# Optimization experiments

Measured on AMD Instinct MI355X. Metric: run time of the kernel, lower is better.

## Reference

```python
import jax, jax.numpy as jnp
import numpy as np

N = 100000
F = 128
H = 128
E = 3200000


def setup_inputs() -> dict:
    key = jax.random.key(0)
    ks = jax.random.split(key, 12)
    s = 1.0 / np.sqrt(F)
    return {
        "x": jax.random.normal(ks[0], (N, F), jnp.float32),
        "edge_weight": jax.random.uniform(ks[1], (E,), jnp.float32),
        "p": jax.random.normal(ks[2], (F,), jnp.float32) * s,
        "w_ih": jax.random.normal(ks[3], (3 * F, F), jnp.float32) * s,
        "w_hh": jax.random.normal(ks[4], (3 * F, F), jnp.float32) * s,
        "b_ih": jax.random.normal(ks[5], (3 * F,), jnp.float32) * s,
        "b_hh": jax.random.normal(ks[6], (3 * F,), jnp.float32) * s,
        "w0": jax.random.normal(ks[7], (F, F), jnp.float32) * s,
        "w_lin": jax.random.normal(ks[8], (H, F), jnp.float32) * s,
        "b_lin": jax.random.normal(ks[9], (H,), jnp.float32) * s,
        "edge_index": jax.random.randint(ks[10], (2, E), 0, N, jnp.int64),
    }


def _evolve_gcnh(x, edge_index, edge_weight, p, w_ih, w_hh, b_ih, b_hh, w0):
    n_nodes, f = x.shape
    # --- TopKPooling: keep k = f nodes by learned projection score ---
    score = jnp.tanh((x @ p) / jnp.linalg.norm(p))  # [N]
    top_scores, idx = jax.lax.top_k(score, f)
    x_tilde = x[idx] * top_scores[:, None]  # [F, F]
    # --- single GRU step (batch=F, input=F): hidden state = GCN weight ---
    gi = x_tilde @ w_ih.T + b_ih  # [F, 3F]
    gh = w0 @ w_hh.T + b_hh       # [F, 3F]
    i_r, i_z, i_n = jnp.split(gi, 3, axis=-1)
    h_r, h_z, h_n = jnp.split(gh, 3, axis=-1)
    r = jax.nn.sigmoid(i_r + h_r)
    z = jax.nn.sigmoid(i_z + h_z)
    n = jnp.tanh(i_n + r * h_n)
    W = (1.0 - z) * n + z * w0  # evolved weight [F, F]
    # --- GCNConv with fixed W: sym-normalized sparse aggregation ---
    src, dst = edge_index[0], edge_index[1]
    loop = jnp.arange(n_nodes)
    src = jnp.concatenate([src, loop])
    dst = jnp.concatenate([dst, loop])
    ew = jnp.concatenate([edge_weight, jnp.ones((n_nodes,), x.dtype)])
    deg = jax.ops.segment_sum(ew, dst, num_segments=n_nodes)
    dinv = jnp.where(deg > 0, jax.lax.rsqrt(deg), 0.0)
    norm = dinv[src] * ew * dinv[dst]  # [E+N]
    xw = x @ W  # [N, F]
    out = jax.ops.segment_sum(norm[:, None] * xw[src], dst, num_segments=n_nodes)
    return out


def reference(x, edge_weight, p, w_ih, w_hh, b_ih, b_hh, w0, w_lin, b_lin, edge_index):
    h = _evolve_gcnh(x, edge_index, edge_weight, p, w_ih, w_hh, b_ih, b_hh, w0)
    h = jax.nn.relu(h)
    return h @ w_lin.T + b_lin
```

## Files before the change

### kernel.cpp

```cpp
#include <hip/hip_runtime.h>
#include <hip/hip_fp16.h>
#include <stdint.h>

#define FD 128
#define CAP 4096
#define PSH 8
#define NPART_MAX 512
#define NBLK1 1024
#define EBUF_MAX 4096
#define SCORE_BLKS 2048
#define TRANS_BLKS 448

static inline size_t alignup256(size_t x) { return (x + 255) & ~(size_t)255; }

struct EdgeP { int s; float w; };

typedef __attribute__((ext_vector_type(4))) float f32x4;
typedef __attribute__((ext_vector_type(8))) short bf16x8;

__device__ __forceinline__ unsigned short f32_to_bf16(float f) {
  unsigned u = __float_as_uint(f);
  u += 0x7fffu + ((u >> 16) & 1u);
  return (unsigned short)(u >> 16);
}
__device__ __forceinline__ unsigned pack_bf16(float a, float b) {
  return ((unsigned)f32_to_bf16(b) << 16) | (unsigned)f32_to_bf16(a);
}
__device__ __forceinline__ unsigned pack_f16(float a, float b) {
  unsigned short ha = __half_as_ushort(__float2half_rn(a));
  unsigned short hb = __half_as_ushort(__float2half_rn(b));
  return ((unsigned)hb << 16) | (unsigned)ha;
}
__device__ __forceinline__ float f16lo(unsigned u) {
  return __half2float(__ushort_as_half((unsigned short)(u & 0xffffu)));
}
__device__ __forceinline__ float f16hi(unsigned u) {
  return __half2float(__ushort_as_half((unsigned short)(u >> 16)));
}
__device__ __forceinline__ unsigned mono32(float f) {
  unsigned u = __float_as_uint(f);
  return (u & 0x80000000u) ? ~u : (u | 0x80000000u);
}
__device__ __forceinline__ unsigned long long mono64(double d) {
  unsigned long long b = (unsigned long long)__double_as_longlong(d);
  return (b & 0x8000000000000000ULL) ? ~b : (b | 0x8000000000000000ULL);
}

__global__ __launch_bounds__(256)
void k_front(const float* __restrict__ x, const float* __restrict__ pvec,
             double* __restrict__ dvals, unsigned* __restrict__ hist,
             unsigned short* __restrict__ xb, unsigned* __restrict__ cnt, int N,
             const int* __restrict__ dstA, unsigned* __restrict__ pcnt, int E, int NPART,
             const float* __restrict__ w_ih, const float* __restrict__ w_hh,
             const float* __restrict__ w_lin, float* __restrict__ w_ihT,
             float* __restrict__ w_hhT, unsigned short* __restrict__ wlb)
{
  int b = blockIdx.x, t = threadIdx.x;
  if (b < SCORE_BLKS) {
    int gid = b * 256 + t;
    if (gid == 0) *cnt = 0u;
    int wid = gid >> 6, lane = t & 63;
    const int nw = (SCORE_BLKS * 256) >> 6;
    double p0 = (double)pvec[lane * 2], p1 = (double)pvec[lane * 2 + 1];
    for (int n = wid; n < N; n += nw) {
      float2 xv = *(const float2*)(x + (size_t)n * FD + lane * 2);
      unsigned pk = pack_f16(xv.x, xv.y);
      *(unsigned*)(xb + (size_t)n * FD + lane * 2) = pk;
      double s = (double)xv.x * p0 + (double)xv.y * p1;
      #pragma unroll
      for (int o = 32; o > 0; o >>= 1) s += __shfl_down(s, o, 64);
      if (lane == 0) {
        dvals[n] = s;
        unsigned u = mono32((float)s);
        atomicAdd(&hist[u >> 16], 1u);
      }
    }
  } else if (b < SCORE_BLKS + NBLK1) {
    __shared__ unsigned lh[NPART_MAX];
    int bid = b - SCORE_BLKS;
    for (int i = t; i < NPART; i += 256) lh[i] = 0;
    __syncthreads();
    int chunk = (E + NBLK1 - 1) / NBLK1;
    int e0 = bid * chunk;
    int e1 = e0 + chunk; if (e1 > E) e1 = E;
    for (int e = e0 + t; e < e1; e += 256)
      atomicAdd(&lh[dstA[e] >> PSH], 1u);
    __syncthreads();
    for (int i = t; i < NPART; i += 256)
      pcnt[(size_t)i * NBLK1 + bid] = lh[i];
  } else {
    int vb = (b - SCORE_BLKS - NBLK1) * 2 + (t >> 7);
    int c = t & 127;
    if (vb < 384)      w_ihT[(size_t)c * 384 + vb]         = w_ih[(size_t)vb * 128 + c];
    else if (vb < 768) w_hhT[(size_t)c * 384 + (vb - 384)] = w_hh[(size_t)(vb - 384) * 128 + c];
    else               wlb[(size_t)(vb - 768) * 128 + c]   = f32_to_bf16(w_lin[(size_t)(vb - 768) * 128 + c]);
  }
}

__global__ __launch_bounds__(1024)
void k_mid1(const unsigned* __restrict__ hist, unsigned* __restrict__ Bthr,
            const unsigned* __restrict__ pcnt, unsigned* __restrict__ basel,
            unsigned* __restrict__ ptot)
{
  int t = threadIdx.x;
  if (blockIdx.x == 0) {
    __shared__ unsigned part[1024];
    unsigned s = 0;
    for (int i = 0; i < 64; i++) s += hist[t * 64 + i];
    part[t] = s;
    __syncthreads();
    if (t == 0) {
      unsigned cum = 0;
      int chunk = 1023;
      for (; chunk >= 0; chunk--) {
        if (cum + part[chunk] >= 128u) break;
        cum += part[chunk];
      }
      unsigned B = 0;
      if (chunk >= 0) {
        int b = chunk * 64 + 63;
        for (; b >= chunk * 64; b--) {
          cum += hist[b];
          if (cum >= 128u) break;
        }
        B = (unsigned)b;
      }
      *Bthr = B;
    }
  } else {
    __shared__ unsigned wtot[16];
    int p = blockIdx.x - 1;
    int lane = t & 63, wv = t >> 6;
    unsigned c = pcnt[(size_t)p * NBLK1 + t];
    unsigned v = c;
    #pragma unroll
    for (int d = 1; d < 64; d <<= 1) {
      unsigned u = __shfl_up(v, d, 64);
      if (lane >= d) v += u;
    }
    if (lane == 63) wtot[wv] = v;
    __syncthreads();
    unsigned add = 0;
    #pragma unroll
    for (int w = 0; w < 16; w++) if (w < wv) add += wtot[w];
    v += add;
    basel[(size_t)p * NBLK1 + t] = v - c;
    if (t == NBLK1 - 1) ptot[p] = v;
  }
}

__global__ __launch_bounds__(512)
void k_mid2(const int* __restrict__ srcA, const int* __restrict__ dstA,
            const float* __restrict__ ew, const unsigned* __restrict__ ptot,
            const unsigned* __restrict__ basel, unsigned long long* __restrict__ epk2,
            int E, int NPART,
            const double* __restrict__ dvals, const unsigned* __restrict__ Bthr,
            unsigned long long* __restrict__ ckey, unsigned* __restrict__ cidx,
            unsigned* __restrict__ cnt, int N)
{
  int t = threadIdx.x;
  if (blockIdx.x < NBLK1) {
    __shared__ unsigned long long ebuf[EBUF_MAX];
    __shared__ unsigned short pbuf[EBUF_MAX];
    __shared__ unsigned lcnt[NPART_MAX];
    __shared__ unsigned lbase[NPART_MAX];
    __shared__ unsigned cur[NPART_MAX];
    __shared__ int gbase[NPART_MAX];
    __shared__ unsigned wt1[8], wt2[8];
    int b = blockIdx.x;
    int chunk = (E + NBLK1 - 1) / NBLK1;
    int e0 = b * chunk;
    int e1 = e0 + chunk; if (e1 > E) e1 = E;
    int n = e1 - e0;

    lcnt[t] = 0;
    unsigned pt = (t < NPART) ? ptot[t] : 0u;
    __syncthreads();
    for (int e = e0 + t; e < e1; e += 512)
      atomicAdd(&lcnt[dstA[e] >> PSH], 1u);
    __syncthreads();
    int lane = t & 63, wv = t >> 6;
    unsigned c1 = lcnt[t];
    unsigned v1 = c1, v2 = pt;
    #pragma unroll
    for (int d = 1; d < 64; d <<= 1) {
      unsigned u1 = __shfl_up(v1, d, 64);
      unsigned u2 = __shfl_up(v2, d, 64);
      if (lane >= d) { v1 += u1; v2 += u2; }
    }
    if (lane == 63) { wt1[wv] = v1; wt2[wv] = v2; }
    __syncthreads();
    unsigned a1 = 0, a2 = 0;
    #pragma unroll
    for (int w = 0; w < 8; w++) if (w < wv) { a1 += wt1[w]; a2 += wt2[w]; }
    v1 += a1; v2 += a2;
    lbase[t] = v1 - c1;
    cur[t] = v1 - c1;
    gbase[t] = (t < NPART) ? ((int)(v2 - pt) + (int)basel[(size_t)t * NBLK1 + b]) : 0;
    __syncthreads();
    for (int e = e0 + t; e < e1; e += 512) {
      int d = dstA[e];
      int s = srcA[e];
      float w = ew[e];
      int p = d >> PSH;
      unsigned long long v = ((unsigned long long)__float_as_uint(w) << 32)
                           | ((unsigned long long)(unsigned)s << 8)
                           | (unsigned long long)(d & 255);
      unsigned pos = atomicAdd(&cur[p], 1u);
      ebuf[pos] = v;
      pbuf[pos] = (unsigned short)p;
    }
    __syncthreads();
    for (int j = t; j < n; j += 512) {
      int p = pbuf[j];
      epk2[gbase[p] + (j - (int)lbase[p])] = ebuf[j];
    }
  } else {
    int i = (blockIdx.x - NBLK1) * 512 + t;
    if (i >= N) return;
    unsigned B = *Bthr;
    double d = dvals[i];
    unsigned u = mono32((float)d);
    if ((u >> 16) >= B) {
      unsigned pos = atomicAdd(cnt, 1u);
      if (pos < CAP) {
        ckey[pos] = ~mono64(d);
        cidx[pos] = (unsigned)i;
      }
    }
  }
}

__global__ __launch_bounds__(512)
void k_mid3(const double* __restrict__ dvals, const float* __restrict__ pvec,
            const unsigned* __restrict__ cnt,
            const unsigned long long* __restrict__ ckey, const unsigned* __restrict__ cidx,
            unsigned* __restrict__ sel_idx, float* __restrict__ sel_ts,
            const unsigned* __restrict__ ptot, const unsigned long long* __restrict__ epk2,
            EdgeP* __restrict__ epk_out, int* __restrict__ off,
            float* __restrict__ dinv, int N, int NPART)
{
  int t = threadIdx.x;
  if (blockIdx.x == 0) {
    __shared__ unsigned long long k[CAP];
    __shared__ unsigned id[CAP];
    __shared__ double red[128];
    __shared__ double pn_sh;
    unsigned C = *cnt;
    if (C > CAP) C = CAP;
    int S = 128;
    while (S < (int)C) S <<= 1;
    for (int i = t; i < S; i += 512) {
      if (i < (int)C) { k[i] = ckey[i]; id[i] = cidx[i]; }
      else            { k[i] = ~0ULL;   id[i] = 0xFFFFFFFFu; }
    }
    __syncthreads();
    for (int kk = 2; kk <= S; kk <<= 1) {
      for (int j = kk >> 1; j > 0; j >>= 1) {
        for (int i = t; i < S; i += 512) {
          int q = i ^ j;
          if (q > i) {
            bool up = ((i & kk) == 0);
            bool g = (k[i] > k[q]) || (k[i] == k[q] && id[i] > id[q]);
            if (g == up) {
              unsigned long long tk = k[i]; k[i] = k[q]; k[q] = tk;
              unsigned ti = id[i]; id[i] = id[q]; id[q] = ti;
            }
          }
        }
        __syncthreads();
      }
    }
    if (t < 128) { double v = (double)pvec[t]; red[t] = v * v; }
    __syncthreads();
    if (t == 0) {
      double s = 0.0;
      for (int i = 0; i < 128; i++) s += red[i];
      pn_sh = sqrt(s);
    }
    __syncthreads();
    if (t < 128) {
      unsigned n = id[t];
      sel_idx[t] = n;
      sel_ts[t] = (float)tanh(dvals[n] / pn_sh);
    }
  } else {
    int p = blockIdx.x - 1;
    int lane = t & 63, wv = t >> 6;
    __shared__ unsigned ws[8];
    __shared__ unsigned wt[4];
    __shared__ unsigned lcnt[256];
    __shared__ float ldeg[256];
    unsigned a = (t < p) ? ptot[t] : 0u;
    #pragma unroll
    for (int d = 32; d > 0; d >>= 1) a += __shfl_xor(a, d, 64);
    if (lane == 0) ws[wv] = a;
    __syncthreads();
    unsigned bu = 0;
    #pragma unroll
    for (int w = 0; w < 8; w++) bu += ws[w];
    int beg = (int)bu;
    int end = beg + (int)ptot[p];

    int n0 = p << PSH;
    int nn = N - n0; if (nn > 256) nn = 256;
    if (t < 256) { lcnt[t] = 0; ldeg[t] = 0.f; }
    __syncthreads();
    for (int i = beg + t; i < end; i += 512) {
      unsigned long long v = epk2[i];
      int ln = (int)(v & 255u);
      float w = __uint_as_float((unsigned)(v >> 32));
      atomicAdd(&lcnt[ln], 1u);
      atomicAdd(&ldeg[ln], w);
    }
    __syncthreads();
    unsigned c = 0, v = 0;
    if (t < 256) {
      c = lcnt[t]; v = c;
      #pragma unroll
      for (int d = 1; d < 64; d <<= 1) {
        unsigned u = __shfl_up(v, d, 64);
        if (lane >= d) v += u;
      }
    }
    if (t < 256 && lane == 63) wt[wv] = v;
    __syncthreads();
    unsigned excl = 0;
    if (t < 256) {
      unsigned add = 0;
      #pragma unroll
      for (int w = 0; w < 4; w++) if (w < wv) add += wt[w];
      v += add;
      excl = v - c;
    }
    if (t < nn) {
      off[n0 + t] = beg + (int)excl;
      dinv[n0 + t] = rsqrtf(ldeg[t] + 1.0f);
    }
    if (p == NPART - 1 && t == 0) off[N] = end;
    if (t < 256) lcnt[t] = excl;
    __syncthreads();
    for (int i = beg + t; i < end; i += 512) {
      unsigned long long vv = epk2[i];
      int ln = (int)(vv & 255u);
      unsigned q = atomicAdd(&lcnt[ln], 1u);
      EdgeP ep;
      ep.s = (int)((vv >> 8) & 0xFFFFFFu);
      ep.w = __uint_as_float((unsigned)(vv >> 32));
      epk_out[beg + (int)q] = ep;
    }
  }
}

__global__ __launch_bounds__(256)
void k_gg(const float* __restrict__ x, const unsigned* __restrict__ sel_idx,
          const float* __restrict__ sel_ts,
          const float* __restrict__ w_ihT, const float* __restrict__ w_hhT,
          const float* __restrict__ b_ih, const float* __restrict__ b_hh,
          const float* __restrict__ w0, unsigned short* __restrict__ WbT,
          const int* __restrict__ off, const EdgeP* __restrict__ epk,
          const float* __restrict__ dinv, const unsigned short* __restrict__ xb,
          unsigned short* __restrict__ aggb, int nbeg, int nend, int ngru)
{
  int t = threadIdx.x;
  if (blockIdx.x < (unsigned)ngru) {
    __shared__ float xt[FD], w0r[FD];
    __shared__ float gi[384], gh[384];
    int i = blockIdx.x;
    if (t < FD) {
      unsigned n = sel_idx[i];
      float ts = sel_ts[i];
      xt[t]  = x[(size_t)n * FD + t] * ts;
      w0r[t] = w0[i * FD + t];
    }
    __syncthreads();
    bool has2 = t < 128;
    float ga0 = b_ih[t], ha0 = b_hh[t];
    float ga1 = 0.f, ha1 = 0.f;
    if (has2) { ga1 = b_ih[256 + t]; ha1 = b_hh[256 + t]; }
    for (int kx = 0; kx < FD; kx++) {
      float xv = xt[kx], hv = w0r[kx];
      const float* wi = w_ihT + (size_t)kx * 384;
      const float* wh = w_hhT + (size_t)kx * 384;
      ga0 += xv * wi[t];
      ha0 += hv * wh[t];
      if (has2) {
        ga1 += xv * wi[256 + t];
        ha1 += hv * wh[256 + t];
      }
    }
    gi[t] = ga0; gh[t] = ha0;
    if (has2) { gi[256 + t] = ga1; gh[256 + t] = ha1; }
    __syncthreads();
    if (t < FD) {
      float r = 1.f / (1.f + expf(-(gi[t] + gh[t])));
      float z = 1.f / (1.f + expf(-(gi[128 + t] + gh[128 + t])));
      float nn = tanhf(gi[256 + t] + r * gh[256 + t]);
      float wv = (1.f - z) * nn + z * w0r[t];
      WbT[(size_t)t * FD + i] = f32_to_bf16(wv);
    }
  } else {
    int gid = (blockIdx.x - ngru) * 256 + t;
    int wid = nbeg + (gid >> 6), lane = t & 63;
    if (wid >= nend) return;
    int g = lane >> 4, sub = lane & 15;
    int n = wid;
    int beg = off[n], end = off[n + 1];
    int cnt = end - beg;
    const EdgeP* ep_base = epk + beg;

    float di = dinv[n];
    uint4 xs4 = *(const uint4*)(xb + (size_t)n * FD + sub * 8);

    float acc[8];
    #pragma unroll
    for (int j = 0; j < 8; j++) acc[j] = 0.f;

    int nfull = cnt >> 4;
    int base = 0;
    for (int s16 = 0; s16 < nfull; s16++, base += 16) {
      uint2 ep[4];
      #pragma unroll
      for (int u = 0; u < 4; u++)
        ep[u] = *(const uint2*)(ep_base + base + u * 4 + g);
      float dv[4]; uint4 pv[4];
      #pragma unroll
      for (int u = 0; u < 4; u++) {
        int s = (int)ep[u].x;
        dv[u] = dinv[s];
        pv[u] = *(const uint4*)(xb + (size_t)s * FD + sub * 8);
      }
      #pragma unroll
      for (int u = 0; u < 4; u++) {
        float w = __uint_as_float(ep[u].y) * dv[u];
        acc[0] = fmaf(f16lo(pv[u].x), w, acc[0]); acc[1] = fmaf(f16hi(pv[u].x), w, acc[1]);
        acc[2] = fmaf(f16lo(pv[u].y), w, acc[2]); acc[3] = fmaf(f16hi(pv[u].y), w, acc[3]);
        acc[4] = fmaf(f16lo(pv[u].z), w, acc[4]); acc[5] = fmaf(f16hi(pv[u].z), w, acc[5]);
        acc[6] = fmaf(f16lo(pv[u].w), w, acc[6]); acc[7] = fmaf(f16hi(pv[u].w), w, acc[7]);
      }
    }
    if (base < cnt) {
      int last = cnt - 1;
      uint2 ep[4];
      #pragma unroll
      for (int u = 0; u < 4; u++) {
        int idx = base + u * 4 + g;
        int idc = idx < cnt ? idx : last;
        ep[u] = *(const uint2*)(ep_base + idc);
      }
      float dv[4]; uint4 pv[4];
      #pragma unroll
      for (int u = 0; u < 4; u++) {
        int s = (int)ep[u].x;
        dv[u] = dinv[s];
        pv[u] = *(const uint4*)(xb + (size_t)s * FD + sub * 8);
      }
      #pragma unroll
      for (int u = 0; u < 4; u++) {
        int idx = base + u * 4 + g;
        float w = (idx < cnt) ? __uint_as_float(ep[u].y) * dv[u] : 0.f;
        acc[0] = fmaf(f16lo(pv[u].x), w, acc[0]); acc[1] = fmaf(f16hi(pv[u].x), w, acc[1]);
        acc[2] = fmaf(f16lo(pv[u].y), w, acc[2]); acc[3] = fmaf(f16hi(pv[u].y), w, acc[3]);
        acc[4] = fmaf(f16lo(pv[u].z), w, acc[4]); acc[5] = fmaf(f16hi(pv[u].z), w, acc[5]);
        acc[6] = fmaf(f16lo(pv[u].w), w, acc[6]); acc[7] = fmaf(f16hi(pv[u].w), w, acc[7]);
      }
    }

    #pragma unroll
    for (int j = 0; j < 8; j++) {
      acc[j] += __shfl_xor(acc[j], 16, 64);
      acc[j] += __shfl_xor(acc[j], 32, 64);
    }
    if (g == 0) {
      float dii = di * di;
      uint4 o;
      o.x = pack_bf16(di * acc[0] + dii * f16lo(xs4.x), di * acc[1] + dii * f16hi(xs4.x));
      o.y = pack_bf16(di * acc[2] + dii * f16lo(xs4.y), di * acc[3] + dii * f16hi(xs4.y));
      o.z = pack_bf16(di * acc[4] + dii * f16lo(xs4.z), di * acc[5] + dii * f16hi(xs4.z));
      o.w = pack_bf16(di * acc[6] + dii * f16lo(xs4.w), di * acc[7] + dii * f16hi(xs4.w));
      *(uint4*)(aggb + (size_t)n * FD + sub * 8) = o;
    }
  }
}

__global__ __launch_bounds__(256)
void gemm_mfma(const unsigned short* __restrict__ aggb, const unsigned short* __restrict__ WbT,
               const unsigned short* __restrict__ wlb, const float* __restrict__ bias,
               float* __restrict__ C, int nrows)
{
  __shared__ unsigned short hs[64][136];
  int tid = threadIdx.x;
  int wv = tid >> 6, lane = tid & 63;
  int row16 = lane & 15;
  int kgrp = lane >> 4;
  int r0 = blockIdx.x * 64;
  int arow = r0 + wv * 16 + row16;
  bool rowok = arow < nrows;

  f32x4 acc[8];
  #pragma unroll
  for (int t = 0; t < 8; t++) acc[t] = (f32x4){0.f, 0.f, 0.f, 0.f};

  #pragma unroll
  for (int ks = 0; ks < 4; ks++) {
    int k = ks * 32 + kgrp * 8;
    bf16x8 a;
    if (rowok) a = *(const bf16x8*)(aggb + (size_t)arow * FD + k);
    else       a = (bf16x8){0, 0, 0, 0, 0, 0, 0, 0};
    #pragma unroll
    for (int t = 0; t < 8; t++) {
      int col = t * 16 + row16;
      bf16x8 b = *(const bf16x8*)(WbT + (size_t)col * FD + k);
      acc[t] = __builtin_amdgcn_mfma_f32_16x16x32_bf16(a, b, acc[t], 0, 0, 0);
    }
  }
  #pragma unroll
  for (int t = 0; t < 8; t++) {
    int col = t * 16 + row16;
    #pragma unroll
    for (int r = 0; r < 4; r++) {
      int row_l = wv * 16 + kgrp * 4 + r;
      hs[row_l][col] = f32_to_bf16(fmaxf(acc[t][r], 0.f));
    }
  }
  __syncthreads();

  f32x4 acc2[8];
  #pragma unroll
  for (int t = 0; t < 8; t++) acc2[t] = (f32x4){0.f, 0.f, 0.f, 0.f};
  #pragma unroll
  for (int ks = 0; ks < 4; ks++) {
    int k = ks * 32 + kgrp * 8;
    bf16x8 a = *(const bf16x8*)(&hs[wv * 16 + row16][k]);
    #pragma unroll
    for (int t = 0; t < 8; t++) {
      int col = t * 16 + row16;
      bf16x8 b = *(const bf16x8*)(wlb + (size_t)col * FD + k);
      acc2[t] = __builtin_amdgcn_mfma_f32_16x16x32_bf16(a, b, acc2[t], 0, 0, 0);
    }
  }
  #pragma unroll
  for (int t = 0; t < 8; t++) {
    int col = t * 16 + row16;
    float bl = bias[col];
    #pragma unroll
    for (int r = 0; r < 4; r++) {
      int row = r0 + wv * 16 + kgrp * 4 + r;
      if (row < nrows) C[(size_t)row * FD + col] = acc2[t][r] + bl;
    }
  }
}

extern "C" void kernel_launch(void* const* d_in, const int* in_sizes, int n_in,
                              void* d_out, int out_size, void* d_ws, size_t ws_size,
                              hipStream_t stream)
{
  const float* x     = (const float*)d_in[0];
  const float* ew    = (const float*)d_in[1];
  const float* pvec  = (const float*)d_in[2];
  const float* w_ih  = (const float*)d_in[3];
  const float* w_hh  = (const float*)d_in[4];
  const float* b_ih  = (const float*)d_in[5];
  const float* b_hh  = (const float*)d_in[6];
  const float* w0    = (const float*)d_in[7];
  const float* w_lin = (const float*)d_in[8];
  const float* b_lin = (const float*)d_in[9];
  const int*   eidx  = (const int*)d_in[10];

  int N = in_sizes[0] / FD;
  int E = in_sizes[1];
  int NPART = (N + 255) >> PSH;
  const int* srcA = eidx;
  const int* dstA = eidx + E;

  char* base = (char*)d_ws;
  size_t off_ws = 0;
  auto take = [&](size_t bytes) -> void* {
    void* ptr = base + off_ws;
    off_ws = alignup256(off_ws + bytes);
    return ptr;
  };
  double* dvals = (double*)take((size_t)N * 8);
  unsigned* hist = (unsigned*)take(65536u * 4);
  unsigned* cnt = (unsigned*)take(4);
  unsigned* Bthr = (unsigned*)take(4);
  unsigned long long* ckey = (unsigned long long*)take((size_t)CAP * 8);
  unsigned* cidx = (unsigned*)take((size_t)CAP * 4);
  unsigned* sel_idx = (unsigned*)take(128 * 4);
  float* sel_ts = (float*)take(128 * 4);
  unsigned short* WbT = (unsigned short*)take(FD * FD * 2);
  unsigned short* wlb = (unsigned short*)take(FD * FD * 2);
  float* w_ihT = (float*)take(3 * FD * FD * 4);
  float* w_hhT = (float*)take(3 * FD * FD * 4);
  float* dinv = (float*)take((size_t)N * 4);
  unsigned* pcnt = (unsigned*)take((size_t)NPART_MAX * NBLK1 * 4);
  unsigned* basel = (unsigned*)take((size_t)NPART_MAX * NBLK1 * 4);
  unsigned* ptot = (unsigned*)take((size_t)NPART_MAX * 4);
  int* off = (int*)take(((size_t)N + 1) * 4);
  unsigned long long* epk2 = (unsigned long long*)take((size_t)E * 8);
  EdgeP* epk_b = (EdgeP*)take((size_t)E * 8);
  unsigned short* xb = (unsigned short*)take((size_t)N * FD * 2);
  unsigned short* aggb = (unsigned short*)take((size_t)N * FD * 2);
  float* out1 = (float*)d_out;

  hipMemsetAsync(hist, 0, 65536u * 4, stream);

  k_front<<<SCORE_BLKS + NBLK1 + TRANS_BLKS, 256, 0, stream>>>(
      x, pvec, dvals, hist, xb, cnt, N, dstA, pcnt, E, NPART,
      w_ih, w_hh, w_lin, w_ihT, w_hhT, wlb);
  k_mid1<<<1 + NPART, 1024, 0, stream>>>(hist, Bthr, pcnt, basel, ptot);
  k_mid2<<<NBLK1 + (N + 511) / 512, 512, 0, stream>>>(
      srcA, dstA, ew, ptot, basel, epk2, E, NPART,
      dvals, Bthr, ckey, cidx, cnt, N);
  k_mid3<<<1 + NPART, 512, 0, stream>>>(
      dvals, pvec, cnt, ckey, cidx, sel_idx, sel_ts,
      ptot, epk2, epk_b, off, dinv, N, NPART);
  int n1 = (N + 2) / 3;
  int n2 = n1 * 2; if (n2 > N) n2 = N;
  k_gg<<<128 + (n1 + 3) / 4, 256, 0, stream>>>(
      x, sel_idx, sel_ts, w_ihT, w_hhT, b_ih, b_hh, w0, WbT,
      off, epk_b, dinv, xb, aggb, 0, n1, 128);
  k_gg<<<(n2 - n1 + 3) / 4, 256, 0, stream>>>(
      x, sel_idx, sel_ts, w_ihT, w_hhT, b_ih, b_hh, w0, WbT,
      off, epk_b, dinv, xb, aggb, n1, n2, 0);
  k_gg<<<(N - n2 + 3) / 4, 256, 0, stream>>>(
      x, sel_idx, sel_ts, w_ihT, w_hhT, b_ih, b_hh, w0, WbT,
      off, epk_b, dinv, xb, aggb, n2, N, 0);
  gemm_mfma<<<(N + 63) / 64, 256, 0, stream>>>(aggb, WbT, wlb, b_lin, out1, N);
}
```

Baseline: 383.4 us.

## Interleave front-kernel branches, unroll scoring, transpose pcnt, merge aggregation launches

The front kernel now interleaves score blocks with edge-histogram blocks, so both memory-bound tasks run side by side instead of being split by block ID range. The scoring loop handles four nodes per wave at a time to expose more loads in flight. The pcnt layout is transposed to block-major so the histogram writes are contiguous, at the cost of strided reads in the scan. The three aggregation launches are merged into one, which removes launch gaps but loses any tail overlap between the separate launches.

```diff
diff --git a/kernel.cpp b/kernel.cpp
--- a/kernel.cpp
+++ b/kernel.cpp
@@ -56,28 +56,50 @@
              float* __restrict__ w_hhT, unsigned short* __restrict__ wlb)
 {
   int b = blockIdx.x, t = threadIdx.x;
-  if (b < SCORE_BLKS) {
-    int gid = b * 256 + t;
+  int branch, bid;
+  if (b < 2 * NBLK1)            { branch = (b & 1); bid = b >> 1; }
+  else if (b < SCORE_BLKS + NBLK1) { branch = 0; bid = NBLK1 + (b - 2 * NBLK1); }
+  else                          { branch = 2; bid = b - (SCORE_BLKS + NBLK1); }
+
+  if (branch == 0) {
+    int gid = bid * 256 + t;
     if (gid == 0) *cnt = 0u;
     int wid = gid >> 6, lane = t & 63;
     const int nw = (SCORE_BLKS * 256) >> 6;
     double p0 = (double)pvec[lane * 2], p1 = (double)pvec[lane * 2 + 1];
-    for (int n = wid; n < N; n += nw) {
-      float2 xv = *(const float2*)(x + (size_t)n * FD + lane * 2);
-      unsigned pk = pack_f16(xv.x, xv.y);
-      *(unsigned*)(xb + (size_t)n * FD + lane * 2) = pk;
-      double s = (double)xv.x * p0 + (double)xv.y * p1;
-      #pragma unroll
-      for (int o = 32; o > 0; o >>= 1) s += __shfl_down(s, o, 64);
+    for (int n0 = wid; n0 < N; n0 += 4 * nw) {
+      int ns[4]; bool ok[4];
+      float2 xv[4];
+      #pragma unroll
+      for (int u = 0; u < 4; u++) {
+        ns[u] = n0 + u * nw;
+        ok[u] = ns[u] < N;
+        xv[u] = make_float2(0.f, 0.f);
+        if (ok[u]) xv[u] = *(const float2*)(x + (size_t)ns[u] * FD + lane * 2);
+      }
+      #pragma unroll
+      for (int u = 0; u < 4; u++)
+        if (ok[u]) *(unsigned*)(xb + (size_t)ns[u] * FD + lane * 2) = pack_f16(xv[u].x, xv[u].y);
+      double s[4];
+      #pragma unroll
+      for (int u = 0; u < 4; u++) s[u] = (double)xv[u].x * p0 + (double)xv[u].y * p1;
+      #pragma unroll
+      for (int o = 32; o > 0; o >>= 1) {
+        #pragma unroll
+        for (int u = 0; u < 4; u++) s[u] += __shfl_down(s[u], o, 64);
+      }
       if (lane == 0) {
-        dvals[n] = s;
-        unsigned u = mono32((float)s);
-        atomicAdd(&hist[u >> 16], 1u);
-      }
-    }
-  } else if (b < SCORE_BLKS + NBLK1) {
+        #pragma unroll
+        for (int u = 0; u < 4; u++) {
+          if (ok[u]) {
+            dvals[ns[u]] = s[u];
+            atomicAdd(&hist[mono32((float)s[u]) >> 16], 1u);
+          }
+        }
+      }
+    }
+  } else if (branch == 1) {
     __shared__ unsigned lh[NPART_MAX];
-    int bid = b - SCORE_BLKS;
     for (int i = t; i < NPART; i += 256) lh[i] = 0;
     __syncthreads();
     int chunk = (E + NBLK1 - 1) / NBLK1;
@@ -87,9 +109,9 @@
       atomicAdd(&lh[dstA[e] >> PSH], 1u);
     __syncthreads();
     for (int i = t; i < NPART; i += 256)
-      pcnt[(size_t)i * NBLK1 + bid] = lh[i];
+      pcnt[(size_t)bid * NPART_MAX + i] = lh[i];
   } else {
-    int vb = (b - SCORE_BLKS - NBLK1) * 2 + (t >> 7);
+    int vb = bid * 2 + (t >> 7);
     int c = t & 127;
     if (vb < 384)      w_ihT[(size_t)c * 384 + vb]         = w_ih[(size_t)vb * 128 + c];
     else if (vb < 768) w_hhT[(size_t)c * 384 + (vb - 384)] = w_hh[(size_t)(vb - 384) * 128 + c];
@@ -131,7 +153,7 @@
     __shared__ unsigned wtot[16];
     int p = blockIdx.x - 1;
     int lane = t & 63, wv = t >> 6;
-    unsigned c = pcnt[(size_t)p * NBLK1 + t];
+    unsigned c = pcnt[(size_t)t * NPART_MAX + p];
     unsigned v = c;
     #pragma unroll
     for (int d = 1; d < 64; d <<= 1) {
@@ -360,10 +382,10 @@
           const float* __restrict__ w0, unsigned short* __restrict__ WbT,
           const int* __restrict__ off, const EdgeP* __restrict__ epk,
           const float* __restrict__ dinv, const unsigned short* __restrict__ xb,
-          unsigned short* __restrict__ aggb, int nbeg, int nend, int ngru)
+          unsigned short* __restrict__ aggb, int N)
 {
   int t = threadIdx.x;
-  if (blockIdx.x < (unsigned)ngru) {
+  if (blockIdx.x < 128) {
     __shared__ float xt[FD], w0r[FD];
     __shared__ float gi[384], gh[384];
     int i = blockIdx.x;
@@ -400,9 +422,9 @@
       WbT[(size_t)t * FD + i] = f32_to_bf16(wv);
     }
   } else {
-    int gid = (blockIdx.x - ngru) * 256 + t;
-    int wid = nbeg + (gid >> 6), lane = t & 63;
-    if (wid >= nend) return;
+    int gid = (blockIdx.x - 128) * 256 + t;
+    int wid = gid >> 6, lane = t & 63;
+    if (wid >= N) return;
     int g = lane >> 4, sub = lane & 15;
     int n = wid;
     int beg = off[n], end = off[n + 1];
@@ -615,16 +637,8 @@
   k_mid3<<<1 + NPART, 512, 0, stream>>>(
       dvals, pvec, cnt, ckey, cidx, sel_idx, sel_ts,
       ptot, epk2, epk_b, off, dinv, N, NPART);
-  int n1 = (N + 2) / 3;
-  int n2 = n1 * 2; if (n2 > N) n2 = N;
-  k_gg<<<128 + (n1 + 3) / 4, 256, 0, stream>>>(
+  k_gg<<<128 + (N * 64 + 255) / 256, 256, 0, stream>>>(
       x, sel_idx, sel_ts, w_ihT, w_hhT, b_ih, b_hh, w0, WbT,
-      off, epk_b, dinv, xb, aggb, 0, n1, 128);
-  k_gg<<<(n2 - n1 + 3) / 4, 256, 0, stream>>>(
-      x, sel_idx, sel_ts, w_ihT, w_hhT, b_ih, b_hh, w0, WbT,
-      off, epk_b, dinv, xb, aggb, n1, n2, 0);
-  k_gg<<<(N - n2 + 3) / 4, 256, 0, stream>>>(
-      x, sel_idx, sel_ts, w_ihT, w_hhT, b_ih, b_hh, w0, WbT,
-      off, epk_b, dinv, xb, aggb, n2, N, 0);
+      off, epk_b, dinv, xb, aggb, N);
   gemm_mfma<<<(N + 63) / 64, 256, 0, stream>>>(aggb, WbT, wlb, b_lin, out1, N);
 }
```

New measurement: 351.9 us. -8.2%, faster.
